# Kernel optimization log

Measured on AMD Instinct MI355X. Metric: run time of the kernel, lower is better.

Reference implementation:

```python
import jax, jax.numpy as jnp
import numpy as np

B, AT, NBR, FEAT = 4, 384, 24, 128


def setup_inputs() -> dict:
    key = jax.random.key(0)
    k1, k2, k3 = jax.random.split(key, 3)
    edge_embedding = jax.random.normal(k1, (B, AT, NBR, FEAT), dtype=jnp.float32)
    nbr_idx = jax.random.randint(k2, (B, AT, NBR), 0, AT, dtype=jnp.int64)
    # periodic-cell offsets: small integers stored as float, compared exactly with ==
    cell_offset = jax.random.randint(k3, (B, AT, NBR, 3), 0, 3).astype(jnp.float32)
    return {"edge_embedding": edge_embedding, "nbr_idx": nbr_idx, "cell_offset": cell_offset}


def reference(edge_embedding, nbr_idx, cell_offset):
    # edge_embedding: (B, At, Nbr, F); nbr_idx: (B, At, Nbr) int; cell_offset: (B, At, Nbr, 3)
    Bn, At, Nbr, F = edge_embedding.shape

    # j_nbr[b,a,j,k] = nbr_idx[b, nbr_idx[b,a,j], k]  -- neighbors of atom j (j-th nbr of a)
    j_nbr = jax.vmap(lambda n: n[n])(nbr_idx)                      # (B, At, Nbr, Nbr)
    # cell_j[b,a,j,k,:] = cell_offset[b, nbr_idx[b,a,j], k, :]
    cell_j = jax.vmap(lambda c, n: c[n])(cell_offset, nbr_idx)     # (B, At, Nbr, Nbr, 3)

    # k_masked[b,a,j,i] = nbr_idx[b,a,i] with diagonal (i==j) set to -1 (exclude k==j)
    eye = jnp.eye(Nbr, dtype=bool)                                 # (Nbr, Nbr) [j, i]
    k_masked = jnp.where(eye[None, None], -1, nbr_idx[:, :, None, :])  # (B, At, Nbr, Nbr)

    # match over k: j_nbr[b,a,j,k] == k_masked[b,a,j,i]
    idx_eq = j_nbr[:, :, :, None, :] == k_masked[:, :, :, :, None]      # (B,At,Nbr,Nbr_i,Nbr_k)
    # cell check: cell_offset[b,a,i,:] == cell_j[b,a,j,k,:] for all 3 coords
    cell_eq = jnp.all(
        cell_offset[:, :, None, :, None, :] == cell_j[:, :, :, None, :, :],
        axis=-1,
    )                                                              # (B,At,Nbr,Nbr_i,Nbr_k)

    mask = jnp.any(idx_eq & cell_eq, axis=-1)                      # (B, At, Nbr_j, Nbr_i)

    # edge_jk[b,a,j,i,:] = edge_embedding[b,a,i,:] where mask else 0
    edge_jk = jnp.where(mask[..., None], edge_embedding[:, :, None, :, :],
                        jnp.zeros((), dtype=edge_embedding.dtype))
    return edge_jk
```

## Files before the change

### kernel.cpp

```cpp
#include <hip/hip_runtime.h>

#define Bb 4
#define AT 384
#define NBR 24
#define FEAT 128
#define ROWQ (FEAT / 4)
#define PANELQ (NBR * ROWQ)

typedef float vfloat4 __attribute__((ext_vector_type(4)));

__global__ __launch_bounds__(256) void mask_kernel(
    const int*   __restrict__ nbr,
    const float* __restrict__ cell,
    unsigned int* __restrict__ ws)
{
    const int ba = blockIdx.x;
    const int b  = ba / AT;
    const int t  = threadIdx.x;

    __shared__ int   s_nbr[NBR];
    __shared__ float s_cell[NBR][3];
    __shared__ int   s_nbrj[NBR][NBR];
    __shared__ float s_cellj[NBR][NBR][3];
    __shared__ int   s_mask[NBR * NBR];

    if (t < NBR) {
        s_nbr[t]     = nbr[ba * NBR + t];
        s_cell[t][0] = cell[(ba * NBR + t) * 3 + 0];
        s_cell[t][1] = cell[(ba * NBR + t) * 3 + 1];
        s_cell[t][2] = cell[(ba * NBR + t) * 3 + 2];
    }
    __syncthreads();

    for (int q = t; q < NBR * NBR; q += 256) {
        const int j = q / NBR;
        const int k = q % NBR;
        const int base = (b * AT + s_nbr[j]) * NBR + k;
        s_nbrj[j][k]     = nbr[base];
        s_cellj[j][k][0] = cell[base * 3 + 0];
        s_cellj[j][k][1] = cell[base * 3 + 1];
        s_cellj[j][k][2] = cell[base * 3 + 2];
    }
    __syncthreads();

    for (int p = t; p < NBR * NBR; p += 256) {
        const int j = p / NBR;
        const int i = p % NBR;
        int m = 0;
        if (i != j) {
            const int   myidx = s_nbr[i];
            const float c0 = s_cell[i][0];
            const float c1 = s_cell[i][1];
            const float c2 = s_cell[i][2];
            #pragma unroll
            for (int k = 0; k < NBR; ++k) {
                if (s_nbrj[j][k] == myidx &&
                    s_cellj[j][k][0] == c0 &&
                    s_cellj[j][k][1] == c1 &&
                    s_cellj[j][k][2] == c2) { m = 1; }
            }
        }
        s_mask[p] = m;
    }
    __syncthreads();

    if (t < NBR) {
        const int j = t;
        unsigned int w = 0;
        #pragma unroll
        for (int i = 0; i < NBR; ++i)
            w |= (unsigned int)s_mask[j * NBR + i] << i;
        ws[ba * NBR + j] = w;
    }
}

__global__ __launch_bounds__(256) void store_kernel(
    const vfloat4* __restrict__ edge,
    const unsigned int* __restrict__ ws,
    vfloat4*       __restrict__ out)
{
    const int blk = blockIdx.x;
    const int ba  = blk / NBR;
    const int t   = threadIdx.x;

    const unsigned int m = ws[blk];

    const vfloat4* __restrict__ erow = edge + (size_t)ba * PANELQ;
    vfloat4*       __restrict__ orow = out  + (size_t)blk * PANELQ;
    const vfloat4 zero = (vfloat4)(0.f);

    #pragma unroll
    for (int it = 0; it < 3; ++it) {
        const int q = it * 256 + t;
        const int i = q >> 5;
        vfloat4 v = zero;
        if ((m >> i) & 1u) v = erow[q];
        __builtin_nontemporal_store(v, &orow[q]);
    }
}

__global__ __launch_bounds__(256) void mono_kernel(
    const float* __restrict__ edge,
    const int*   __restrict__ nbr,
    const float* __restrict__ cell,
    float*       __restrict__ out)
{
    const int blk = blockIdx.x;
    const int j   = blk % NBR;
    const int ba  = blk / NBR;
    const int b   = ba / AT;

    __shared__ int   s_nbrj[NBR];
    __shared__ float s_cellj[NBR][3];
    __shared__ int   s_mask[NBR];

    const int t = threadIdx.x;
    const int jatom = nbr[ba * NBR + j];

    if (t < NBR) {
        const int base = (b * AT + jatom) * NBR + t;
        s_nbrj[t]     = nbr[base];
        s_cellj[t][0] = cell[base * 3 + 0];
        s_cellj[t][1] = cell[base * 3 + 1];
        s_cellj[t][2] = cell[base * 3 + 2];
    }
    __syncthreads();

    if (t < NBR) {
        const int i = t;
        int m = 0;
        if (i != j) {
            const int   myidx = nbr[ba * NBR + i];
            const float c0 = cell[(ba * NBR + i) * 3 + 0];
            const float c1 = cell[(ba * NBR + i) * 3 + 1];
            const float c2 = cell[(ba * NBR + i) * 3 + 2];
            #pragma unroll
            for (int k = 0; k < NBR; ++k) {
                if (s_nbrj[k] == myidx &&
                    s_cellj[k][0] == c0 &&
                    s_cellj[k][1] == c1 &&
                    s_cellj[k][2] == c2) { m = 1; }
            }
        }
        s_mask[i] = m;
    }
    __syncthreads();

    const float4* __restrict__ erow = (const float4*)(edge + (size_t)ba * NBR * FEAT);
    float4*       __restrict__ orow = (float4*)(out + (size_t)blk * NBR * FEAT);
    const float4 zero = make_float4(0.f, 0.f, 0.f, 0.f);
    #pragma unroll
    for (int it = 0; it < 3; ++it) {
        const int q = t + it * 256;
        const int i = q >> 5;
        float4 v = zero;
        if (s_mask[i]) v = erow[q];
        orow[q] = v;
    }
}

extern "C" void kernel_launch(void* const* d_in, const int* in_sizes, int n_in,
                              void* d_out, int out_size, void* d_ws, size_t ws_size,
                              hipStream_t stream) {
    const float* edge = (const float*)d_in[0];
    const int*   nbr  = (const int*)d_in[1];
    const float* cell = (const float*)d_in[2];
    float*       out  = (float*)d_out;

    const size_t need = (size_t)Bb * AT * NBR * sizeof(unsigned int);
    if (ws_size >= need) {
        unsigned int* ws = (unsigned int*)d_ws;
        mask_kernel<<<Bb * AT, 256, 0, stream>>>(nbr, cell, ws);
        store_kernel<<<Bb * AT * NBR, 256, 0, stream>>>((const vfloat4*)edge, ws,
                                                        (vfloat4*)out);
    } else {
        mono_kernel<<<Bb * AT * NBR, 256, 0, stream>>>(edge, nbr, cell, out);
    }
}
```

Baseline: 95.05 us.

## Use grid-stride persistent store kernel with wave-uniform mask and normal stores

```diff
diff --git a/kernel.cpp b/kernel.cpp
--- a/kernel.cpp
+++ b/kernel.cpp
@@ -5,7 +5,9 @@
 #define NBR 24
 #define FEAT 128
 #define ROWQ (FEAT / 4)
-#define PANELQ (NBR * ROWQ)
+#define TILEQ (NBR * ROWQ)
+#define NTILES (Bb * AT * NBR)
+#define OUTQ ((unsigned)NTILES * TILEQ)
 
 typedef float vfloat4 __attribute__((ext_vector_type(4)));
 
@@ -65,12 +67,11 @@
     __syncthreads();
 
     if (t < NBR) {
-        const int j = t;
         unsigned int w = 0;
         #pragma unroll
         for (int i = 0; i < NBR; ++i)
-            w |= (unsigned int)s_mask[j * NBR + i] << i;
-        ws[ba * NBR + j] = w;
+            w |= (unsigned int)s_mask[t * NBR + i] << i;
+        ws[ba * NBR + t] = w;
     }
 }
 
@@ -79,23 +80,23 @@
     const unsigned int* __restrict__ ws,
     vfloat4*       __restrict__ out)
 {
-    const int blk = blockIdx.x;
-    const int ba  = blk / NBR;
-    const int t   = threadIdx.x;
+    const vfloat4 zero = (vfloat4)(0.f);
+    const unsigned stride = gridDim.x * 256u;
+    unsigned q = blockIdx.x * 256u + threadIdx.x;
 
-    const unsigned int m = ws[blk];
-
-    const vfloat4* __restrict__ erow = edge + (size_t)ba * PANELQ;
-    vfloat4*       __restrict__ orow = out  + (size_t)blk * PANELQ;
-    const vfloat4 zero = (vfloat4)(0.f);
-
-    #pragma unroll
-    for (int it = 0; it < 3; ++it) {
-        const int q = it * 256 + t;
-        const int i = q >> 5;
+    for (; q < OUTQ; q += stride) {
+        const unsigned tile   = q / TILEQ;
+        const unsigned within = q - tile * TILEQ;
+        const unsigned w = __builtin_amdgcn_readfirstlane(ws[tile]);
         vfloat4 v = zero;
-        if ((m >> i) & 1u) v = erow[q];
-        __builtin_nontemporal_store(v, &orow[q]);
+        if (w) {
+            const unsigned i = within >> 5;
+            if ((w >> i) & 1u) {
+                const unsigned ba = tile / NBR;
+                v = edge[(size_t)ba * TILEQ + within];
+            }
+        }
+        out[q] = v;
     }
 }
 
@@ -127,13 +128,12 @@
     __syncthreads();
 
     if (t < NBR) {
-        const int i = t;
         int m = 0;
-        if (i != j) {
-            const int   myidx = nbr[ba * NBR + i];
-            const float c0 = cell[(ba * NBR + i) * 3 + 0];
-            const float c1 = cell[(ba * NBR + i) * 3 + 1];
-            const float c2 = cell[(ba * NBR + i) * 3 + 2];
+        if (t != j) {
+            const int   myidx = nbr[ba * NBR + t];
+            const float c0 = cell[(ba * NBR + t) * 3 + 0];
+            const float c1 = cell[(ba * NBR + t) * 3 + 1];
+            const float c2 = cell[(ba * NBR + t) * 3 + 2];
             #pragma unroll
             for (int k = 0; k < NBR; ++k) {
                 if (s_nbrj[k] == myidx &&
@@ -142,7 +142,7 @@
                     s_cellj[k][2] == c2) { m = 1; }
             }
         }
-        s_mask[i] = m;
+        s_mask[t] = m;
     }
     __syncthreads();
 
@@ -167,13 +167,13 @@
     const float* cell = (const float*)d_in[2];
     float*       out  = (float*)d_out;
 
-    const size_t need = (size_t)Bb * AT * NBR * sizeof(unsigned int);
+    const size_t need = (size_t)NTILES * sizeof(unsigned int);
     if (ws_size >= need) {
         unsigned int* ws = (unsigned int*)d_ws;
         mask_kernel<<<Bb * AT, 256, 0, stream>>>(nbr, cell, ws);
-        store_kernel<<<Bb * AT * NBR, 256, 0, stream>>>((const vfloat4*)edge, ws,
-                                                        (vfloat4*)out);
+        store_kernel<<<2048, 256, 0, stream>>>((const vfloat4*)edge, ws,
+                                               (vfloat4*)out);
     } else {
-        mono_kernel<<<Bb * AT * NBR, 256, 0, stream>>>(edge, nbr, cell, out);
+        mono_kernel<<<NTILES, 256, 0, stream>>>(edge, nbr, cell, out);
     }
 }
```

Result: slower. 103.1 us (+8.4%).
